# Kernel tuning notes

Measured on AMD Instinct MI355X. Metric: run time of the kernel, lower is better.

## Reference

```python
import jax, jax.numpy as jnp
import numpy as np

NUM_HEADS = 8
NUM_GROUPS = 32
EPS = 1e-5


def group_norm(x, gamma, beta):
    B, C, H, W = x.shape
    xg = x.reshape(B, NUM_GROUPS, C // NUM_GROUPS * H * W)
    mean = xg.mean(axis=-1, keepdims=True)
    var = xg.var(axis=-1, keepdims=True)
    xg = (xg - mean) * jax.lax.rsqrt(var + EPS)
    xn = xg.reshape(B, C, H, W)
    return xn * gamma[None, :, None, None] + beta[None, :, None, None]


def setup_inputs() -> dict:
    key = jax.random.key(0)
    ks = jax.random.split(key, 7)
    C = 512
    B, H, W = 8, 32, 32
    x = jax.random.normal(ks[0], (B, C, H, W), dtype=jnp.float32)
    gamma = jnp.ones((C,), dtype=jnp.float32)
    beta = jnp.zeros((C,), dtype=jnp.float32)
    # 1x1 conv weights stored as [out, in]
    w_qkv = jax.random.normal(ks[1], (3 * C, C), dtype=jnp.float32) * (1.0 / np.sqrt(C))
    b_qkv = jax.random.normal(ks[2], (3 * C,), dtype=jnp.float32) * 0.02
    w_proj = jax.random.normal(ks[3], (C, C), dtype=jnp.float32) * (1.0 / np.sqrt(C))
    b_proj = jax.random.normal(ks[4], (C,), dtype=jnp.float32) * 0.02
    return {"x": x, "gamma": gamma, "beta": beta, "w_qkv": w_qkv,
            "b_qkv": b_qkv, "w_proj": w_proj, "b_proj": b_proj}


def reference(x, gamma, beta, w_qkv, b_qkv, w_proj, b_proj):
    B, C, H, W = x.shape
    hd = C // NUM_HEADS  # head_dim
    x_norm = group_norm(x, gamma, beta)
    # 1x1 conv: [B,C,H,W] x [3C,C] -> [B,3C,H,W]
    qkv = jnp.einsum('bchw,oc->bohw', x_norm, w_qkv) + b_qkv[None, :, None, None]
    q, k, v = jnp.split(qkv, 3, axis=1)
    N = H * W
    q = q.reshape(B, NUM_HEADS, hd, N)
    k = k.reshape(B, NUM_HEADS, hd, N)
    v = v.reshape(B, NUM_HEADS, hd, N)
    attn = jnp.einsum('bhcn,bhcm->bhnm', q, k) * (hd ** -0.5)
    attn = jax.nn.softmax(attn, axis=-1)
    out = jnp.einsum('bhnm,bhcm->bhcn', attn, v)
    out = out.reshape(B, C, H, W)
    proj = jnp.einsum('bchw,oc->bohw', out, w_proj) + b_proj[None, :, None, None]
    return x + proj
```

## Files before the change

kernel.cpp:

```cpp
#include <hip/hip_runtime.h>
#include <hip/hip_bf16.h>

#define BB 8
#define CC 512
#define NN 1024
#define NG 32
#define CPG 16
#define NH 8
#define HD 64
#define C3 1536
#define QKLD 1024

typedef __hip_bfloat16 bf16;
typedef unsigned short ushort_t;

typedef __attribute__((ext_vector_type(8))) short bf16x8;
typedef __attribute__((ext_vector_type(8))) unsigned short ushortx8;
typedef __attribute__((ext_vector_type(4))) float floatx4;

__device__ __forceinline__ float b2f(bf16 h) { return __bfloat162float(h); }
__device__ __forceinline__ bf16 f2b(float f) { return __float2bfloat16(f); }
__device__ __forceinline__ float us2f(ushort_t u) {
    union { unsigned int i; float f; } c; c.i = ((unsigned int)u) << 16; return c.f;
}
__device__ __forceinline__ ushort_t f2us(float f) {
    bf16 h = __float2bfloat16(f);
    return *(ushort_t*)&h;
}

__global__ __launch_bounds__(256) void gn_kernel(const float* __restrict__ x,
                                                 const float* __restrict__ gamma,
                                                 const float* __restrict__ beta,
                                                 bf16* __restrict__ xnT) {
    const int GSZ = CPG * NN;
    int b = blockIdx.x >> 5;
    int g = blockIdx.x & 31;
    size_t base = ((size_t)b * CC + (size_t)g * CPG) * NN;
    int tid = threadIdx.x;
    float s = 0.f, s2 = 0.f;
    for (int i = tid; i < GSZ; i += 256) {
        float v = x[base + i];
        s += v; s2 += v * v;
    }
#pragma unroll
    for (int off = 32; off > 0; off >>= 1) {
        s  += __shfl_down(s, off, 64);
        s2 += __shfl_down(s2, off, 64);
    }
    __shared__ float rs[4], rs2[4], stat[2];
    __shared__ ushort_t Lt[16][264];
    int wid = tid >> 6, lane = tid & 63;
    if (lane == 0) { rs[wid] = s; rs2[wid] = s2; }
    __syncthreads();
    if (tid == 0) {
        float ts  = rs[0] + rs[1] + rs[2] + rs[3];
        float ts2 = rs2[0] + rs2[1] + rs2[2] + rs2[3];
        float mean = ts * (1.f / GSZ);
        float var  = ts2 * (1.f / GSZ) - mean * mean;
        stat[0] = mean;
        stat[1] = rsqrtf(var + 1e-5f);
    }
    __syncthreads();
    float mean = stat[0], inv = stat[1];

    int c_loc = tid >> 4;
    int nsp   = (tid & 15) * 16;
    float ga = gamma[g * CPG + c_loc];
    float be = beta[g * CPG + c_loc];
    const float* srcrow = x + base + (size_t)c_loc * NN;

    for (int nc = 0; nc < 4; ++nc) {
        int nb = nc * 256 + nsp;
        float fv[16];
        *(float4*)(fv + 0)  = *(const float4*)(srcrow + nb + 0);
        *(float4*)(fv + 4)  = *(const float4*)(srcrow + nb + 4);
        *(float4*)(fv + 8)  = *(const float4*)(srcrow + nb + 8);
        *(float4*)(fv + 12) = *(const float4*)(srcrow + nb + 12);
        ushortx8 u0, u1;
#pragma unroll
        for (int j = 0; j < 8; ++j) {
            u0[j] = f2us((fv[j]     - mean) * inv * ga + be);
            u1[j] = f2us((fv[j + 8] - mean) * inv * ga + be);
        }
        *(ushortx8*)&Lt[c_loc][nsp]     = u0;
        *(ushortx8*)&Lt[c_loc][nsp + 8] = u1;
        __syncthreads();
        ushort_t o16[16];
#pragma unroll
        for (int c = 0; c < 16; ++c) o16[c] = Lt[c][tid];
        ushort_t* dst = (ushort_t*)xnT + ((size_t)b * NN + nc * 256 + tid) * CC + g * CPG;
        *(uint4*)dst       = *(const uint4*)(o16);
        *(uint4*)(dst + 8) = *(const uint4*)(o16 + 8);
        __syncthreads();
    }
}

#define GSTR 40
__global__ __launch_bounds__(256) void qkv_gemm(const bf16* __restrict__ xnT,
                                                const float* __restrict__ w,
                                                const float* __restrict__ bias,
                                                bf16* __restrict__ qkT,
                                                bf16* __restrict__ vN) {
    __shared__ ushort_t Wl[128 * GSTR];
    __shared__ ushort_t Xl[128 * GSTR];
    int b  = blockIdx.z;
    int o0 = blockIdx.y * 128;
    int n0 = blockIdx.x * 128;
    int tid = threadIdx.x;
    int wv = tid >> 6, ln = tid & 15, qd = (tid >> 4) & 3;
    int wm = wv >> 1, wn = wv & 1;

    int srow = tid >> 1;
    int kh   = (tid & 1) * 16;
    const float* wp = w + (size_t)(o0 + srow) * CC;
    const ushort_t* xp = (const ushort_t*)xnT + ((size_t)b * NN + n0 + srow) * CC;

    floatx4 acc[4][4];
#pragma unroll
    for (int i = 0; i < 4; ++i)
#pragma unroll
        for (int j = 0; j < 4; ++j) acc[i][j] = (floatx4){0.f, 0.f, 0.f, 0.f};

    float fw[16];
    uint4 xr0, xr1;
    *(float4*)(fw + 0)  = *(const float4*)(wp + kh + 0);
    *(float4*)(fw + 4)  = *(const float4*)(wp + kh + 4);
    *(float4*)(fw + 8)  = *(const float4*)(wp + kh + 8);
    *(float4*)(fw + 12) = *(const float4*)(wp + kh + 12);
    xr0 = *(const uint4*)(xp + kh);
    xr1 = *(const uint4*)(xp + kh + 8);

    for (int k0 = 0; k0 < CC; k0 += 32) {
        {
            ushortx8 u0, u1;
#pragma unroll
            for (int j = 0; j < 8; ++j) { u0[j] = f2us(fw[j]); u1[j] = f2us(fw[j + 8]); }
            *(ushortx8*)&Wl[srow * GSTR + kh]     = u0;
            *(ushortx8*)&Wl[srow * GSTR + kh + 8] = u1;
            *(uint4*)&Xl[srow * GSTR + kh]     = xr0;
            *(uint4*)&Xl[srow * GSTR + kh + 8] = xr1;
        }
        __syncthreads();
        if (k0 + 32 < CC) {
            int kn = k0 + 32;
            *(float4*)(fw + 0)  = *(const float4*)(wp + kn + kh + 0);
            *(float4*)(fw + 4)  = *(const float4*)(wp + kn + kh + 4);
            *(float4*)(fw + 8)  = *(const float4*)(wp + kn + kh + 8);
            *(float4*)(fw + 12) = *(const float4*)(wp + kn + kh + 12);
            xr0 = *(const uint4*)(xp + kn + kh);
            xr1 = *(const uint4*)(xp + kn + kh + 8);
        }
        bf16x8 af[4], bfr[4];
#pragma unroll
        for (int i = 0; i < 4; ++i)
            af[i] = *(const bf16x8*)&Wl[(wm * 64 + i * 16 + ln) * GSTR + qd * 8];
#pragma unroll
        for (int j = 0; j < 4; ++j)
            bfr[j] = *(const bf16x8*)&Xl[(wn * 64 + j * 16 + ln) * GSTR + qd * 8];
#pragma unroll
        for (int i = 0; i < 4; ++i)
#pragma unroll
            for (int j = 0; j < 4; ++j)
                acc[i][j] = __builtin_amdgcn_mfma_f32_16x16x32_bf16(af[i], bfr[j], acc[i][j], 0, 0, 0);
        __syncthreads();
    }

    if (o0 < 1024) {
#pragma unroll
        for (int i = 0; i < 4; ++i) {
            int ob = o0 + wm * 64 + i * 16 + qd * 4;
            float sc = (ob < 512) ? 0.18033688011112042f : 1.0f;
#pragma unroll
            for (int j = 0; j < 4; ++j) {
                int n = n0 + wn * 64 + j * 16 + ln;
                ushort_t pk[4];
#pragma unroll
                for (int r = 0; r < 4; ++r)
                    pk[r] = f2us((acc[i][j][r] + bias[ob + r]) * sc);
                *(uint2*)((ushort_t*)qkT + ((size_t)b * NN + n) * QKLD + ob) = *(uint2*)pk;
            }
        }
    } else {
#pragma unroll
        for (int i = 0; i < 4; ++i) {
#pragma unroll
            for (int r = 0; r < 4; ++r) {
                int o = o0 + wm * 64 + i * 16 + qd * 4 + r;
                float bb = bias[o];
                size_t rb = ((size_t)b * CC + (o - 1024)) * NN + n0 + wn * 64 + ln;
#pragma unroll
                for (int j = 0; j < 4; ++j)
                    vN[rb + j * 16] = f2b(acc[i][j][r] + bb);
            }
        }
    }
}

__global__ __launch_bounds__(256, 4) void attn_kernel(const bf16* __restrict__ qkTp,
                                                      const bf16* __restrict__ vNp,
                                                      bf16* __restrict__ aoT) {
    __shared__ ushort_t Kt[2][64 * 64];
    __shared__ ushort_t Vn[2][64 * 64];
    __shared__ ushort_t Pw[4][16 * 64];

    int h  = blockIdx.x;
    int qt = blockIdx.y;
    int bi = blockIdx.z;
    int q0 = qt * 64;
    int tid = threadIdx.x;
    int wq = tid >> 6;
    int l  = tid & 63;
    int ln = l & 15;
    int qd = (l >> 4) & 3;
    int l7 = ln & 7;
    int lb = ln >> 3;

    const ushort_t* qkT = (const ushort_t*)qkTp;
    const ushort_t* vN  = (const ushort_t*)vNp;

    const ushort_t* qsrc = qkT + ((size_t)bi * NN + q0 + wq * 16 + ln) * QKLD + h * HD + qd * 8;
    bf16x8 aq0 = *(const bf16x8*)(qsrc);
    bf16x8 aq1 = *(const bf16x8*)(qsrc + 32);

    bf16x8 ones;
#pragma unroll
    for (int j = 0; j < 8; ++j) ones[j] = (short)0x3F80;

    floatx4 O[4];
#pragma unroll
    for (int t = 0; t < 4; ++t) O[t] = (floatx4){0.f, 0.f, 0.f, 0.f};
    floatx4 lsum = (floatx4){0.f, 0.f, 0.f, 0.f};

    ushort_t* Pme = &Pw[wq][0];

    int ksl0 = (qd ^ l7) * 8;
    int ksl1 = ((qd + 4) ^ l7) * 8;

    int srow = tid >> 2;
    int g1   = tid & 3;
    int s7   = srow & 7;
    int ko1  = (g1 ^ s7) * 8;
    int ko2  = ((g1 + 4) ^ s7) * 8;
    const ushort_t* ks = qkT + ((size_t)bi * NN + srow) * QKLD + 512 + h * HD + g1 * 8;
    const ushort_t* vs = vN + ((size_t)bi * CC + h * HD + srow) * NN + g1 * 8;

    uint4 kr0 = *(const uint4*)(ks);
    uint4 kr1 = *(const uint4*)(ks + 32);
    uint4 vr0 = *(const uint4*)(vs);
    uint4 vr1 = *(const uint4*)(vs + 32);
    {
        ushort_t* kd = &Kt[0][srow * 64];
        *(uint4*)(kd + ko1) = kr0; *(uint4*)(kd + ko2) = kr1;
        ushort_t* vd = &Vn[0][srow * 64];
        *(uint4*)(vd + ko1) = vr0; *(uint4*)(vd + ko2) = vr1;
    }
    kr0 = *(const uint4*)(ks + (size_t)64 * QKLD);
    kr1 = *(const uint4*)(ks + (size_t)64 * QKLD + 32);
    vr0 = *(const uint4*)(vs + 64);
    vr1 = *(const uint4*)(vs + 64 + 32);
    __syncthreads();

    for (int it = 0; it < 16; ++it) {
        int cur = it & 1;
        const ushort_t* KtC = &Kt[cur][0];
        const ushort_t* VnC = &Vn[cur][0];
        if (it < 15) {
            ushort_t* kd = &Kt[cur ^ 1][srow * 64];
            *(uint4*)(kd + ko1) = kr0; *(uint4*)(kd + ko2) = kr1;
            ushort_t* vd = &Vn[cur ^ 1][srow * 64];
            *(uint4*)(vd + ko1) = vr0; *(uint4*)(vd + ko2) = vr1;
        }
        if (it < 14) {
            size_t mo = (size_t)(it + 2) * 64;
            kr0 = *(const uint4*)(ks + mo * QKLD);
            kr1 = *(const uint4*)(ks + mo * QKLD + 32);
            vr0 = *(const uint4*)(vs + mo);
            vr1 = *(const uint4*)(vs + mo + 32);
        }

        floatx4 S[4];
#pragma unroll
        for (int t = 0; t < 4; ++t) {
            const ushort_t* krow = KtC + (t * 16 + ln) * 64;
            bf16x8 b0 = *(const bf16x8*)(krow + ksl0);
            bf16x8 b1 = *(const bf16x8*)(krow + ksl1);
            floatx4 acc = (floatx4){0.f, 0.f, 0.f, 0.f};
            acc = __builtin_amdgcn_mfma_f32_16x16x32_bf16(aq0, b0, acc, 0, 0, 0);
            acc = __builtin_amdgcn_mfma_f32_16x16x32_bf16(aq1, b1, acc, 0, 0, 0);
            S[t] = acc;
        }

#pragma unroll
        for (int t = 0; t < 4; ++t) {
#pragma unroll
            for (int r = 0; r < 4; ++r) {
                float p = exp2f(S[t][r]);
                int qr = qd * 4 + r;
                Pme[qr * 64 + ((t * 2 + lb) ^ (qr & 7)) * 8 + l7] = f2us(p);
            }
        }
        bf16x8 pa0 = *(const bf16x8*)&Pme[ln * 64 + ksl0];
        bf16x8 pa1 = *(const bf16x8*)&Pme[ln * 64 + ksl1];

        lsum = __builtin_amdgcn_mfma_f32_16x16x32_bf16(pa0, ones, lsum, 0, 0, 0);
        lsum = __builtin_amdgcn_mfma_f32_16x16x32_bf16(pa1, ones, lsum, 0, 0, 0);

#pragma unroll
        for (int t = 0; t < 4; ++t) {
            const ushort_t* vrow = VnC + (t * 16 + ln) * 64;
            bf16x8 v0 = *(const bf16x8*)(vrow + ksl0);
            bf16x8 v1 = *(const bf16x8*)(vrow + ksl1);
            O[t] = __builtin_amdgcn_mfma_f32_16x16x32_bf16(pa0, v0, O[t], 0, 0, 0);
            O[t] = __builtin_amdgcn_mfma_f32_16x16x32_bf16(pa1, v1, O[t], 0, 0, 0);
        }
        if (it < 15) __syncthreads();
    }

    float inv[4];
#pragma unroll
    for (int r = 0; r < 4; ++r) inv[r] = 1.f / lsum[r];
#pragma unroll
    for (int t = 0; t < 4; ++t) {
#pragma unroll
        for (int r = 0; r < 4; ++r) {
            int n = q0 + wq * 16 + qd * 4 + r;
            ((ushort_t*)aoT)[((size_t)bi * NN + n) * CC + h * HD + t * 16 + ln] =
                f2us(O[t][r] * inv[r]);
        }
    }
}

__global__ __launch_bounds__(256) void proj_gemm(const bf16* __restrict__ aoT,
                                                 const float* __restrict__ w,
                                                 const float* __restrict__ bias,
                                                 const float* __restrict__ xres,
                                                 float* __restrict__ out) {
    __shared__ ushort_t Wl[64 * GSTR];
    __shared__ ushort_t Xl[128 * GSTR];
    int b  = blockIdx.z;
    int o0 = blockIdx.y * 64;
    int n0 = blockIdx.x * 128;
    int tid = threadIdx.x;
    int wv = tid >> 6, ln = tid & 15, qd = (tid >> 4) & 3;
    int wm = wv >> 1, wn = wv & 1;

    int srow = tid >> 1;
    int kh   = (tid & 1) * 16;
    const ushort_t* xp = (const ushort_t*)aoT + ((size_t)b * NN + n0 + srow) * CC;
    const float* wp = w + (size_t)(o0 + (srow & 63)) * CC;
    bool doW = (tid < 128);

    floatx4 acc[2][4];
#pragma unroll
    for (int i = 0; i < 2; ++i)
#pragma unroll
        for (int j = 0; j < 4; ++j) acc[i][j] = (floatx4){0.f, 0.f, 0.f, 0.f};

    float fw[16];
    uint4 xr0, xr1;
    if (doW) {
        *(float4*)(fw + 0)  = *(const float4*)(wp + kh + 0);
        *(float4*)(fw + 4)  = *(const float4*)(wp + kh + 4);
        *(float4*)(fw + 8)  = *(const float4*)(wp + kh + 8);
        *(float4*)(fw + 12) = *(const float4*)(wp + kh + 12);
    }
    xr0 = *(const uint4*)(xp + kh);
    xr1 = *(const uint4*)(xp + kh + 8);

    for (int k0 = 0; k0 < CC; k0 += 32) {
        if (doW) {
            ushortx8 u0, u1;
#pragma unroll
            for (int j = 0; j < 8; ++j) { u0[j] = f2us(fw[j]); u1[j] = f2us(fw[j + 8]); }
            *(ushortx8*)&Wl[(srow & 63) * GSTR + kh]     = u0;
            *(ushortx8*)&Wl[(srow & 63) * GSTR + kh + 8] = u1;
        }
        *(uint4*)&Xl[srow * GSTR + kh]     = xr0;
        *(uint4*)&Xl[srow * GSTR + kh + 8] = xr1;
        __syncthreads();
        if (k0 + 32 < CC) {
            int kn = k0 + 32;
            if (doW) {
                *(float4*)(fw + 0)  = *(const float4*)(wp + kn + kh + 0);
                *(float4*)(fw + 4)  = *(const float4*)(wp + kn + kh + 4);
                *(float4*)(fw + 8)  = *(const float4*)(wp + kn + kh + 8);
                *(float4*)(fw + 12) = *(const float4*)(wp + kn + kh + 12);
            }
            xr0 = *(const uint4*)(xp + kn + kh);
            xr1 = *(const uint4*)(xp + kn + kh + 8);
        }
        bf16x8 af[2], bfr[4];
#pragma unroll
        for (int i = 0; i < 2; ++i)
            af[i] = *(const bf16x8*)&Wl[(wm * 32 + i * 16 + ln) * GSTR + qd * 8];
#pragma unroll
        for (int j = 0; j < 4; ++j)
            bfr[j] = *(const bf16x8*)&Xl[(wn * 64 + j * 16 + ln) * GSTR + qd * 8];
#pragma unroll
        for (int i = 0; i < 2; ++i)
#pragma unroll
            for (int j = 0; j < 4; ++j)
                acc[i][j] = __builtin_amdgcn_mfma_f32_16x16x32_bf16(af[i], bfr[j], acc[i][j], 0, 0, 0);
        __syncthreads();
    }

#pragma unroll
    for (int i = 0; i < 2; ++i) {
#pragma unroll
        for (int r = 0; r < 4; ++r) {
            int o = o0 + wm * 32 + i * 16 + qd * 4 + r;
            float bb = bias[o];
            size_t rb = ((size_t)b * CC + o) * NN + n0 + wn * 64 + ln;
#pragma unroll
            for (int j = 0; j < 4; ++j)
                out[rb + j * 16] = acc[i][j][r] + bb + xres[rb + j * 16];
        }
    }
}

extern "C" void kernel_launch(void* const* d_in, const int* in_sizes, int n_in,
                              void* d_out, int out_size, void* d_ws, size_t ws_size,
                              hipStream_t stream) {
    const float* x      = (const float*)d_in[0];
    const float* gamma  = (const float*)d_in[1];
    const float* beta   = (const float*)d_in[2];
    const float* w_qkv  = (const float*)d_in[3];
    const float* b_qkv  = (const float*)d_in[4];
    const float* w_proj = (const float*)d_in[5];
    const float* b_proj = (const float*)d_in[6];
    float* out = (float*)d_out;

    bf16* xnT = (bf16*)d_ws;
    bf16* qkT = xnT + (size_t)BB * CC * NN;
    bf16* vN  = qkT + (size_t)BB * NN * QKLD;
    bf16* aoT = xnT;

    gn_kernel<<<BB * NG, 256, 0, stream>>>(x, gamma, beta, xnT);
    qkv_gemm<<<dim3(NN / 128, C3 / 128, BB), 256, 0, stream>>>(xnT, w_qkv, b_qkv, qkT, vN);
    attn_kernel<<<dim3(NH, NN / 64, BB), 256, 0, stream>>>(qkT, vN, aoT);
    proj_gemm<<<dim3(NN / 128, CC / 64, BB), 256, 0, stream>>>(aoT, w_proj, b_proj, x, out);
}
```

Measured before the change: 182.8 us.

## Pre-convert weights to bf16 in GN kernel; use K=64 swizzled LDS tiles in GEMMs

Sixteen extra blocks in the group-norm kernel convert the qkv and proj weights from fp32 to bf16 once per call. Each GEMM then loads bf16 weights directly instead of reading fp32 and converting per tile. The GEMM K-step grows from 32 to 64, and the padded LDS layout is replaced by an XOR swizzle to avoid bank conflicts. This halves weight traffic and the number of barriers, at the cost of more LDS per block and extra work in the GN launch.

Result: slower. 241.5 us (+32.2%).

```diff
diff --git a/kernel.cpp b/kernel.cpp
--- a/kernel.cpp
+++ b/kernel.cpp
@@ -31,12 +31,33 @@
 __global__ __launch_bounds__(256) void gn_kernel(const float* __restrict__ x,
                                                  const float* __restrict__ gamma,
                                                  const float* __restrict__ beta,
-                                                 bf16* __restrict__ xnT) {
+                                                 bf16* __restrict__ xnT,
+                                                 const float* __restrict__ wqkv,
+                                                 const float* __restrict__ wproj,
+                                                 ushort_t* __restrict__ wqkvB,
+                                                 ushort_t* __restrict__ wprojB) {
+    int tid = threadIdx.x;
+    if (blockIdx.x >= 256) {
+        int wb = blockIdx.x - 256;
+        int base = (wb * 256 + tid) * 4;
+        const int STR = 16 * 256 * 4;
+        for (int i = base; i < C3 * CC; i += STR) {
+            float4 f = *(const float4*)(wqkv + i);
+            ushort_t u[4] = {f2us(f.x), f2us(f.y), f2us(f.z), f2us(f.w)};
+            *(uint2*)(wqkvB + i) = *(uint2*)u;
+        }
+        for (int i = base; i < CC * CC; i += STR) {
+            float4 f = *(const float4*)(wproj + i);
+            ushort_t u[4] = {f2us(f.x), f2us(f.y), f2us(f.z), f2us(f.w)};
+            *(uint2*)(wprojB + i) = *(uint2*)u;
+        }
+        return;
+    }
+
     const int GSZ = CPG * NN;
     int b = blockIdx.x >> 5;
     int g = blockIdx.x & 31;
     size_t base = ((size_t)b * CC + (size_t)g * CPG) * NN;
-    int tid = threadIdx.x;
     float s = 0.f, s2 = 0.f;
     for (int i = tid; i < GSZ; i += 256) {
         float v = x[base + i];
@@ -95,25 +116,26 @@
     }
 }
 
-#define GSTR 40
-__global__ __launch_bounds__(256) void qkv_gemm(const bf16* __restrict__ xnT,
-                                                const float* __restrict__ w,
+__global__ __launch_bounds__(256) void qkv_gemm(const ushort_t* __restrict__ wB,
+                                                const bf16* __restrict__ xnT,
                                                 const float* __restrict__ bias,
                                                 bf16* __restrict__ qkT,
                                                 bf16* __restrict__ vN) {
-    __shared__ ushort_t Wl[128 * GSTR];
-    __shared__ ushort_t Xl[128 * GSTR];
+    __shared__ ushort_t Wl[128 * 64];
+    __shared__ ushort_t Xl[128 * 64];
     int b  = blockIdx.z;
     int o0 = blockIdx.y * 128;
     int n0 = blockIdx.x * 128;
     int tid = threadIdx.x;
     int wv = tid >> 6, ln = tid & 15, qd = (tid >> 4) & 3;
     int wm = wv >> 1, wn = wv & 1;
-
-    int srow = tid >> 1;
-    int kh   = (tid & 1) * 16;
-    const float* wp = w + (size_t)(o0 + srow) * CC;
-    const ushort_t* xp = (const ushort_t*)xnT + ((size_t)b * NN + n0 + srow) * CC;
+    int l7 = ln & 7;
+
+    int sr = tid >> 1;
+    int gb = (tid & 1) * 4;
+    int s7 = sr & 7;
+    const ushort_t* wp = wB + (size_t)(o0 + sr) * CC + gb * 8;
+    const ushort_t* xp = (const ushort_t*)xnT + ((size_t)b * NN + n0 + sr) * CC + gb * 8;
 
     floatx4 acc[4][4];
 #pragma unroll
@@ -121,47 +143,44 @@
 #pragma unroll
         for (int j = 0; j < 4; ++j) acc[i][j] = (floatx4){0.f, 0.f, 0.f, 0.f};
 
-    float fw[16];
-    uint4 xr0, xr1;
-    *(float4*)(fw + 0)  = *(const float4*)(wp + kh + 0);
-    *(float4*)(fw + 4)  = *(const float4*)(wp + kh + 4);
-    *(float4*)(fw + 8)  = *(const float4*)(wp + kh + 8);
-    *(float4*)(fw + 12) = *(const float4*)(wp + kh + 12);
-    xr0 = *(const uint4*)(xp + kh);
-    xr1 = *(const uint4*)(xp + kh + 8);
-
-    for (int k0 = 0; k0 < CC; k0 += 32) {
-        {
-            ushortx8 u0, u1;
-#pragma unroll
-            for (int j = 0; j < 8; ++j) { u0[j] = f2us(fw[j]); u1[j] = f2us(fw[j + 8]); }
-            *(ushortx8*)&Wl[srow * GSTR + kh]     = u0;
-            *(ushortx8*)&Wl[srow * GSTR + kh + 8] = u1;
-            *(uint4*)&Xl[srow * GSTR + kh]     = xr0;
-            *(uint4*)&Xl[srow * GSTR + kh + 8] = xr1;
-        }
-        __syncthreads();
-        if (k0 + 32 < CC) {
-            int kn = k0 + 32;
-            *(float4*)(fw + 0)  = *(const float4*)(wp + kn + kh + 0);
-            *(float4*)(fw + 4)  = *(const float4*)(wp + kn + kh + 4);
-            *(float4*)(fw + 8)  = *(const float4*)(wp + kn + kh + 8);
-            *(float4*)(fw + 12) = *(const float4*)(wp + kn + kh + 12);
-            xr0 = *(const uint4*)(xp + kn + kh);
-            xr1 = *(const uint4*)(xp + kn + kh + 8);
-        }
-        bf16x8 af[4], bfr[4];
-#pragma unroll
-        for (int i = 0; i < 4; ++i)
-            af[i] = *(const bf16x8*)&Wl[(wm * 64 + i * 16 + ln) * GSTR + qd * 8];
-#pragma unroll
-        for (int j = 0; j < 4; ++j)
-            bfr[j] = *(const bf16x8*)&Xl[(wn * 64 + j * 16 + ln) * GSTR + qd * 8];
-#pragma unroll
-        for (int i = 0; i < 4; ++i)
+    uint4 wr[4], xr[4];
+#pragma unroll
+    for (int i = 0; i < 4; ++i) {
+        wr[i] = *(const uint4*)(wp + i * 8);
+        xr[i] = *(const uint4*)(xp + i * 8);
+    }
+
+    for (int k0 = 0; k0 < CC; k0 += 64) {
+#pragma unroll
+        for (int i = 0; i < 4; ++i) {
+            int gs = (gb + i) ^ s7;
+            *(uint4*)&Wl[sr * 64 + gs * 8] = wr[i];
+            *(uint4*)&Xl[sr * 64 + gs * 8] = xr[i];
+        }
+        __syncthreads();
+        if (k0 + 64 < CC) {
+#pragma unroll
+            for (int i = 0; i < 4; ++i) {
+                wr[i] = *(const uint4*)(wp + k0 + 64 + i * 8);
+                xr[i] = *(const uint4*)(xp + k0 + 64 + i * 8);
+            }
+        }
+#pragma unroll
+        for (int kk = 0; kk < 2; ++kk) {
+            bf16x8 af[4], bfr[4];
+            int go = ((kk * 4 + qd) ^ l7) * 8;
+#pragma unroll
+            for (int i = 0; i < 4; ++i)
+                af[i] = *(const bf16x8*)&Wl[(wm * 64 + i * 16 + ln) * 64 + go];
 #pragma unroll
             for (int j = 0; j < 4; ++j)
-                acc[i][j] = __builtin_amdgcn_mfma_f32_16x16x32_bf16(af[i], bfr[j], acc[i][j], 0, 0, 0);
+                bfr[j] = *(const bf16x8*)&Xl[(wn * 64 + j * 16 + ln) * 64 + go];
+#pragma unroll
+            for (int i = 0; i < 4; ++i)
+#pragma unroll
+                for (int j = 0; j < 4; ++j)
+                    acc[i][j] = __builtin_amdgcn_mfma_f32_16x16x32_bf16(af[i], bfr[j], acc[i][j], 0, 0, 0);
+        }
         __syncthreads();
     }
 
@@ -331,23 +350,26 @@
 }
 
 __global__ __launch_bounds__(256) void proj_gemm(const bf16* __restrict__ aoT,
-                                                 const float* __restrict__ w,
+                                                 const ushort_t* __restrict__ wB,
                                                  const float* __restrict__ bias,
                                                  const float* __restrict__ xres,
                                                  float* __restrict__ out) {
-    __shared__ ushort_t Wl[64 * GSTR];
-    __shared__ ushort_t Xl[128 * GSTR];
+    __shared__ ushort_t Wl[64 * 64];
+    __shared__ ushort_t Xl[128 * 64];
     int b  = blockIdx.z;
     int o0 = blockIdx.y * 64;
     int n0 = blockIdx.x * 128;
     int tid = threadIdx.x;
     int wv = tid >> 6, ln = tid & 15, qd = (tid >> 4) & 3;
     int wm = wv >> 1, wn = wv & 1;
-
-    int srow = tid >> 1;
-    int kh   = (tid & 1) * 16;
-    const ushort_t* xp = (const ushort_t*)aoT + ((size_t)b * NN + n0 + srow) * CC;
-    const float* wp = w + (size_t)(o0 + (srow & 63)) * CC;
+    int l7 = ln & 7;
+
+    int sr = tid >> 1;
+    int gb = (tid & 1) * 4;
+    int s7 = sr & 7;
+    const ushort_t* xp = (const ushort_t*)aoT + ((size_t)b * NN + n0 + sr) * CC + gb * 8;
+    int wsr = (tid >> 1) & 63;
+    const ushort_t* wp = wB + (size_t)(o0 + wsr) * CC + gb * 8;
     bool doW = (tid < 128);
 
     floatx4 acc[2][4];
@@ -356,51 +378,47 @@
 #pragma unroll
         for (int j = 0; j < 4; ++j) acc[i][j] = (floatx4){0.f, 0.f, 0.f, 0.f};
 
-    float fw[16];
-    uint4 xr0, xr1;
-    if (doW) {
-        *(float4*)(fw + 0)  = *(const float4*)(wp + kh + 0);
-        *(float4*)(fw + 4)  = *(const float4*)(wp + kh + 4);
-        *(float4*)(fw + 8)  = *(const float4*)(wp + kh + 8);
-        *(float4*)(fw + 12) = *(const float4*)(wp + kh + 12);
-    }
-    xr0 = *(const uint4*)(xp + kh);
-    xr1 = *(const uint4*)(xp + kh + 8);
-
-    for (int k0 = 0; k0 < CC; k0 += 32) {
-        if (doW) {
-            ushortx8 u0, u1;
-#pragma unroll
-            for (int j = 0; j < 8; ++j) { u0[j] = f2us(fw[j]); u1[j] = f2us(fw[j + 8]); }
-            *(ushortx8*)&Wl[(srow & 63) * GSTR + kh]     = u0;
-            *(ushortx8*)&Wl[(srow & 63) * GSTR + kh + 8] = u1;
-        }
-        *(uint4*)&Xl[srow * GSTR + kh]     = xr0;
-        *(uint4*)&Xl[srow * GSTR + kh + 8] = xr1;
-        __syncthreads();
-        if (k0 + 32 < CC) {
-            int kn = k0 + 32;
+    uint4 wr[4], xr[4];
+#pragma unroll
+    for (int i = 0; i < 4; ++i) {
+        xr[i] = *(const uint4*)(xp + i * 8);
+        if (doW) wr[i] = *(const uint4*)(wp + i * 8);
+    }
+
+    for (int k0 = 0; k0 < CC; k0 += 64) {
+#pragma unroll
+        for (int i = 0; i < 4; ++i) {
+            int gs = (gb + i) ^ s7;
+            *(uint4*)&Xl[sr * 64 + gs * 8] = xr[i];
             if (doW) {
-                *(float4*)(fw + 0)  = *(const float4*)(wp + kn + kh + 0);
-                *(float4*)(fw + 4)  = *(const float4*)(wp + kn + kh + 4);
-                *(float4*)(fw + 8)  = *(const float4*)(wp + kn + kh + 8);
-                *(float4*)(fw + 12) = *(const float4*)(wp + kn + kh + 12);
-            }
-            xr0 = *(const uint4*)(xp + kn + kh);
-            xr1 = *(const uint4*)(xp + kn + kh + 8);
-        }
-        bf16x8 af[2], bfr[4];
-#pragma unroll
-        for (int i = 0; i < 2; ++i)
-            af[i] = *(const bf16x8*)&Wl[(wm * 32 + i * 16 + ln) * GSTR + qd * 8];
-#pragma unroll
-        for (int j = 0; j < 4; ++j)
-            bfr[j] = *(const bf16x8*)&Xl[(wn * 64 + j * 16 + ln) * GSTR + qd * 8];
-#pragma unroll
-        for (int i = 0; i < 2; ++i)
+                int gw = (gb + i) ^ (wsr & 7);
+                *(uint4*)&Wl[wsr * 64 + gw * 8] = wr[i];
+            }
+        }
+        __syncthreads();
+        if (k0 + 64 < CC) {
+#pragma unroll
+            for (int i = 0; i < 4; ++i) {
+                xr[i] = *(const uint4*)(xp + k0 + 64 + i * 8);
+                if (doW) wr[i] = *(const uint4*)(wp + k0 + 64 + i * 8);
+            }
+        }
+#pragma unroll
+        for (int kk = 0; kk < 2; ++kk) {
+            bf16x8 af[2], bfr[4];
+            int go = ((kk * 4 + qd) ^ l7) * 8;
+#pragma unroll
+            for (int i = 0; i < 2; ++i)
+                af[i] = *(const bf16x8*)&Wl[(wm * 32 + i * 16 + ln) * 64 + go];
 #pragma unroll
             for (int j = 0; j < 4; ++j)
-                acc[i][j] = __builtin_amdgcn_mfma_f32_16x16x32_bf16(af[i], bfr[j], acc[i][j], 0, 0, 0);
+                bfr[j] = *(const bf16x8*)&Xl[(wn * 64 + j * 16 + ln) * 64 + go];
+#pragma unroll
+            for (int i = 0; i < 2; ++i)
+#pragma unroll
+                for (int j = 0; j < 4; ++j)
+                    acc[i][j] = __builtin_amdgcn_mfma_f32_16x16x32_bf16(af[i], bfr[j], acc[i][j], 0, 0, 0);
+        }
         __syncthreads();
     }
 
@@ -433,10 +451,13 @@
     bf16* xnT = (bf16*)d_ws;
     bf16* qkT = xnT + (size_t)BB * CC * NN;
     bf16* vN  = qkT + (size_t)BB * NN * QKLD;
+    ushort_t* wqkvB  = (ushort_t*)(vN + (size_t)BB * CC * NN);
+    ushort_t* wprojB = wqkvB + (size_t)C3 * CC;
     bf16* aoT = xnT;
 
-    gn_kernel<<<BB * NG, 256, 0, stream>>>(x, gamma, beta, xnT);
-    qkv_gemm<<<dim3(NN / 128, C3 / 128, BB), 256, 0, stream>>>(xnT, w_qkv, b_qkv, qkT, vN);
+    gn_kernel<<<BB * NG + 16, 256, 0, stream>>>(x, gamma, beta, xnT,
+                                                w_qkv, w_proj, wqkvB, wprojB);
+    qkv_gemm<<<dim3(NN / 128, C3 / 128, BB), 256, 0, stream>>>(wqkvB, xnT, b_qkv, qkT, vN);
     attn_kernel<<<dim3(NH, NN / 64, BB), 256, 0, stream>>>(qkT, vN, aoT);
-    proj_gemm<<<dim3(NN / 128, CC / 64, BB), 256, 0, stream>>>(aoT, w_proj, b_proj, x, out);
-}
+    proj_gemm<<<dim3(NN / 128, CC / 64, BB), 256, 0, stream>>>(aoT, wprojB, b_proj, x, out);
+}
```
